# Performance work log

Measured on AMD Instinct MI355X. Metric: run time of the kernel, lower is better.

## Reference

```python
import jax, jax.numpy as jnp
import numpy as np

NBIT = 4          # weight bit-width
GROUP_SIZE = 128  # weight quantization group size (divides k)
HAS_WEIGHT_ZEROS = True


def _quant_dequant_weights(w, group_size=GROUP_SIZE, nbit=NBIT, has_zeros=HAS_WEIGHT_ZEROS):
    # Mirrors torchao _quantize + quantize_per_channel_group, then dequantizes
    # (the native kernel dequantizes inline with the matmul; math is identical).
    qmin = -(1 << (nbit - 1))
    qmax = (1 << (nbit - 1)) - 1
    n, k = w.shape
    g = w.reshape(-1, group_size)                      # [n*k/gs, gs]
    vmin = g.min(axis=1, keepdims=True)
    vmax = g.max(axis=1, keepdims=True)
    scales = (vmax - vmin) / (qmax - qmin)             # per-group scale
    if has_zeros:
        zeros = qmin - jnp.round(vmin / scales)
    else:
        zeros = jnp.zeros_like(scales)
    q = jnp.clip(jnp.round(g / scales) + zeros, qmin, qmax)
    deq = (q - zeros) * scales
    return deq.reshape(n, k)


def _dyn_quant_dequant_act(x):
    # Dynamic per-token (per-row) asymmetric int8 activation quantization.
    qmin, qmax = -128, 127
    xmin = x.min(axis=-1, keepdims=True)
    xmax = x.max(axis=-1, keepdims=True)
    scale = (xmax - xmin) / (qmax - qmin)
    zero = qmin - jnp.round(xmin / scale)
    q = jnp.clip(jnp.round(x / scale) + zero, qmin, qmax)
    return (q - zero) * scale


def setup_inputs() -> dict:
    key = jax.random.key(0)
    k1, k2 = jax.random.split(key)
    x = jax.random.normal(k1, (4, 2048, 4096), dtype=jnp.float32)
    weights = jax.random.normal(k2, (4096, 4096), dtype=jnp.float32) * 0.02
    return {"x": x, "weights": weights}


def reference(x, weights):
    w_deq = _quant_dequant_weights(weights)            # [n, k]
    x_deq = _dyn_quant_dequant_act(x)                  # [..., m, k]
    # y[..., m, n] = x_deq @ w_deq^T
    return jnp.einsum('bmk,nk->bmn', x_deq, w_deq)
```

## Files before the change

kernel.cpp:

```cpp
#include <hip/hip_runtime.h>
#include <hip/hip_bf16.h>
#include <cfloat>

typedef __attribute__((ext_vector_type(8))) short bf16x8;
typedef __attribute__((ext_vector_type(4))) float f32x4;

#define M_DIM 8192
#define N_DIM 4096
#define K_DIM 4096

__device__ inline ushort f2bf(float f) {
    unsigned u = __float_as_uint(f);
    unsigned r = (u + 0x7FFFu + ((u >> 16) & 1u)) >> 16;
    return (ushort)r;
}

#define SWZ(x) ((x) ^ ((((x) >> 7) & 7) << 4))

__global__ __launch_bounds__(256) void w_dequant(const float* __restrict__ w,
                                                 ushort* __restrict__ wq) {
    int g = blockIdx.x * 4 + (threadIdx.x >> 6);
    int lane = threadIdx.x & 63;
    const float* src = w + (size_t)g * 128;
    float2 v = *(const float2*)(src + lane * 2);
    float mn = fminf(v.x, v.y), mx = fmaxf(v.x, v.y);
#pragma unroll
    for (int s = 1; s < 64; s <<= 1) {
        mn = fminf(mn, __shfl_xor(mn, s));
        mx = fmaxf(mx, __shfl_xor(mx, s));
    }
    float scale = (mx - mn) / 15.0f;
    float zero  = -8.0f - rintf(mn / scale);
    float q0 = fminf(fmaxf(rintf(v.x / scale) + zero, -8.0f), 7.0f);
    float q1 = fminf(fmaxf(rintf(v.y / scale) + zero, -8.0f), 7.0f);
    ushort2 o;
    o.x = f2bf((q0 - zero) * scale);
    o.y = f2bf((q1 - zero) * scale);
    *(ushort2*)(wq + (size_t)g * 128 + lane * 2) = o;
}

__global__ __launch_bounds__(256) void act_qdq(const float* __restrict__ x,
                                               ushort* __restrict__ xq) {
    __shared__ float smn[4], smx[4];
    int row = blockIdx.x;
    const float* xr = x + (size_t)row * K_DIM;
    ushort* xo = xq + (size_t)row * K_DIM;
    int t = threadIdx.x;
    float4 v[4];
    float mn = FLT_MAX, mx = -FLT_MAX;
#pragma unroll
    for (int i = 0; i < 4; i++) {
        v[i] = ((const float4*)xr)[t + i * 256];
        mn = fminf(mn, fminf(fminf(v[i].x, v[i].y), fminf(v[i].z, v[i].w)));
        mx = fmaxf(mx, fmaxf(fmaxf(v[i].x, v[i].y), fmaxf(v[i].z, v[i].w)));
    }
#pragma unroll
    for (int s = 1; s < 64; s <<= 1) {
        mn = fminf(mn, __shfl_xor(mn, s));
        mx = fmaxf(mx, __shfl_xor(mx, s));
    }
    int w = t >> 6;
    if ((t & 63) == 0) { smn[w] = mn; smx[w] = mx; }
    __syncthreads();
    mn = fminf(fminf(smn[0], smn[1]), fminf(smn[2], smn[3]));
    mx = fmaxf(fmaxf(smx[0], smx[1]), fmaxf(smx[2], smx[3]));
    float scale = (mx - mn) / 255.0f;
    float zero  = -128.0f - rintf(mn / scale);
#pragma unroll
    for (int i = 0; i < 4; i++) {
        float e0 = v[i].x, e1 = v[i].y, e2 = v[i].z, e3 = v[i].w;
        ushort4 o;
        float q;
        q = fminf(fmaxf(rintf(e0 / scale) + zero, -128.0f), 127.0f); o.x = f2bf((q - zero) * scale);
        q = fminf(fmaxf(rintf(e1 / scale) + zero, -128.0f), 127.0f); o.y = f2bf((q - zero) * scale);
        q = fminf(fmaxf(rintf(e2 / scale) + zero, -128.0f), 127.0f); o.z = f2bf((q - zero) * scale);
        q = fminf(fmaxf(rintf(e3 / scale) + zero, -128.0f), 127.0f); o.w = f2bf((q - zero) * scale);
        ((ushort4*)xo)[t + i * 256] = o;
    }
}

#define BM 256
#define BN 256
#define BK 64
#define NT (K_DIM / BK)
#define HH(T, q) (4 * (T) + (q))

__global__ __launch_bounds__(512, 1) void gemm_bt8(const ushort* __restrict__ A,
                                                   const ushort* __restrict__ B,
                                                   float* __restrict__ C) {
    __shared__ __align__(16) ushort As[2][BM * BK];
    __shared__ __align__(16) ushort Bs[2][BN * BK];

    const int nbx = N_DIM / BN;
    const int nwg = (M_DIM / BM) * nbx;
    int bid = blockIdx.x;
    bid = (bid & 7) * (nwg / 8) + (bid >> 3);
    int mb = bid / nbx, nb = bid % nbx;
    size_t m0 = (size_t)mb * BM, n0 = (size_t)nb * BN;

    const int t = threadIdx.x;
    const int w = t >> 6, lane = t & 63;
    const int wm = w >> 2, wn = w & 3;
    const int lr = lane & 15;
    const int lk = (lane >> 4) << 3;

    const ushort* Ab = A + m0 * K_DIM;
    const ushort* Bb = B + n0 * K_DIM;

    auto STAGE = [&](int h) {
        if (h < 0 || h >= NT * 4) return;
        int T = h >> 2, q = h & 3;
        int d = T & 1;
        ushort* reg = (q < 2) ? As[d] : Bs[d];
        const ushort* gbase = (q < 2) ? Ab : Bb;
        int rhalf = q & 1;
        int k0 = T * BK;
#pragma unroll
        for (int l = 0; l < 2; l++) {
            int base = rhalf * 16384 + (w * 2 + l) * 1024;
            int lb = base + lane * 16;
            int lg = SWZ(lb);
            int r = lg >> 7;
            int c = (lg & 127) >> 1;
            __builtin_amdgcn_global_load_lds(
                (const __attribute__((address_space(1))) unsigned int*)(gbase + (size_t)r * K_DIM + k0 + c),
                (__attribute__((address_space(3))) unsigned int*)((char*)reg + base),
                16, 0, 0);
        }
    };

    f32x4 acc[8][4] = {};
    bf16x8 afr[2][2], bfr[4][2];

#define PHASE(d, q, hA, hB, vm) do {                                              \
    if ((q) == 0) {                                                               \
        _Pragma("unroll") for (int ni = 0; ni < 4; ni++)                          \
        _Pragma("unroll") for (int kk = 0; kk < 2; kk++) {                        \
            int row = wn * 64 + ni * 16 + lr;                                     \
            int lg = row * 128 + (kk * 32 + lk) * 2;                              \
            int pb = SWZ(lg);                                                     \
            bfr[ni][kk] = *(const bf16x8*)((const char*)Bs[d] + pb);              \
        }                                                                         \
    }                                                                             \
    _Pragma("unroll") for (int ii = 0; ii < 2; ii++)                              \
    _Pragma("unroll") for (int kk = 0; kk < 2; kk++) {                            \
        int row = wm * 128 + ((q) * 2 + ii) * 16 + lr;                            \
        int lg = row * 128 + (kk * 32 + lk) * 2;                                  \
        int pb = SWZ(lg);                                                         \
        afr[ii][kk] = *(const bf16x8*)((const char*)As[d] + pb);                  \
    }                                                                             \
    STAGE(hA);                                                                    \
    STAGE(hB);                                                                    \
    __builtin_amdgcn_s_barrier();                                                 \
    asm volatile("s_waitcnt lgkmcnt(0)" ::: "memory");                            \
    __builtin_amdgcn_sched_barrier(0);                                            \
    __builtin_amdgcn_s_setprio(1);                                                \
    _Pragma("unroll") for (int ii = 0; ii < 2; ii++)                              \
    _Pragma("unroll") for (int ni = 0; ni < 4; ni++)                              \
    _Pragma("unroll") for (int kk = 0; kk < 2; kk++)                              \
        acc[(q) * 2 + ii][ni] = __builtin_amdgcn_mfma_f32_16x16x32_bf16(          \
            afr[ii][kk], bfr[ni][kk], acc[(q) * 2 + ii][ni], 0, 0, 0);            \
    __builtin_amdgcn_s_setprio(0);                                                \
    if ((vm) == 1) asm volatile("s_waitcnt vmcnt(4)" ::: "memory");               \
    if ((vm) == 2) asm volatile("s_waitcnt vmcnt(0)" ::: "memory");               \
    __builtin_amdgcn_s_barrier();                                                 \
  } while (0)

    STAGE(HH(0, 0)); STAGE(HH(0, 1)); STAGE(HH(0, 2)); STAGE(HH(0, 3));
    STAGE(HH(1, 2)); STAGE(HH(1, 3));
    asm volatile("s_waitcnt vmcnt(4)" ::: "memory");
    __builtin_amdgcn_s_barrier();

#pragma unroll 1
    for (int i = 0; i < NT / 2 - 1; i++) {
        int T2 = 2 * i;
        PHASE(0, 0, HH(T2 + 1, 0), -1,             0);
        PHASE(0, 1, HH(T2 + 1, 1), HH(T2 + 2, 2),  0);
        PHASE(0, 2, HH(T2 + 2, 3), -1,             0);
        PHASE(0, 3, -1, -1,                        1);
        PHASE(1, 0, HH(T2 + 2, 0), -1,             0);
        PHASE(1, 1, HH(T2 + 2, 1), HH(T2 + 3, 2),  0);
        PHASE(1, 2, HH(T2 + 3, 3), -1,             0);
        PHASE(1, 3, -1, -1,                        1);
    }

    PHASE(0, 0, HH(NT - 1, 0), -1, 0);
    PHASE(0, 1, HH(NT - 1, 1), -1, 0);
    PHASE(0, 2, -1, -1, 0);
    PHASE(0, 3, -1, -1, 2);
    PHASE(1, 0, -1, -1, 0);
    PHASE(1, 1, -1, -1, 0);
    PHASE(1, 2, -1, -1, 0);
    PHASE(1, 3, -1, -1, 0);
#undef PHASE

    int fq = lane >> 4;
#pragma unroll
    for (int mi = 0; mi < 8; mi++) {
#pragma unroll
        for (int ni = 0; ni < 4; ni++) {
#pragma unroll
            for (int r = 0; r < 4; r++) {
                size_t crow = m0 + wm * 128 + mi * 16 + fq * 4 + r;
                C[crow * N_DIM + n0 + wn * 64 + ni * 16 + lr] = acc[mi][ni][r];
            }
        }
    }
}

extern "C" void kernel_launch(void* const* d_in, const int* in_sizes, int n_in,
                              void* d_out, int out_size, void* d_ws, size_t ws_size,
                              hipStream_t stream) {
    const float* x = (const float*)d_in[0];
    const float* w = (const float*)d_in[1];
    float* out = (float*)d_out;

    ushort* wq = (ushort*)d_ws;
    ushort* xq = (ushort*)((char*)d_ws + (size_t)N_DIM * K_DIM * 2);

    hipLaunchKernelGGL(w_dequant, dim3((N_DIM * K_DIM / 128) / 4), dim3(256), 0, stream, w, wq);
    hipLaunchKernelGGL(act_qdq, dim3(M_DIM), dim3(256), 0, stream, x, xq);
    hipLaunchKernelGGL(gemm_bt8, dim3((M_DIM / BM) * (N_DIM / BN)), dim3(512), 0, stream, xq, wq, out);
}
```

Baseline: 330.5 us.

## Re-slice GEMM LDS staging into quarter chunks and interleave A rows across waves

Splits each global-to-LDS tile load into eight smaller chunks (four for A, four for B), issues two of them in every compute phase, and waits with vmcnt at the end of every phase instead of only every fourth one. It also remaps each wave's A rows so that phase q reads a 64-row slab shared by both wave rows, so a phase only depends on the A quarter already loaded. The aim is to spread memory traffic evenly across phases and start MFMA work on partially loaded tiles. The cost is more frequent waitcnt stalls and tighter ordering that could expose load latency.

Measured after the change: 327.1 us. About the same (-1.0%).

```diff
diff --git a/kernel.cpp b/kernel.cpp
--- a/kernel.cpp
+++ b/kernel.cpp
@@ -83,7 +83,6 @@
 #define BN 256
 #define BK 64
 #define NT (K_DIM / BK)
-#define HH(T, q) (4 * (T) + (q))
 
 __global__ __launch_bounds__(512, 1) void gemm_bt8(const ushort* __restrict__ A,
                                                    const ushort* __restrict__ B,
@@ -107,32 +106,28 @@
     const ushort* Ab = A + m0 * K_DIM;
     const ushort* Bb = B + n0 * K_DIM;
 
-    auto STAGE = [&](int h) {
-        if (h < 0 || h >= NT * 4) return;
-        int T = h >> 2, q = h & 3;
+    auto STAGE = [&](int T, int qq) {
+        if (T >= NT) return;
         int d = T & 1;
-        ushort* reg = (q < 2) ? As[d] : Bs[d];
-        const ushort* gbase = (q < 2) ? Ab : Bb;
-        int rhalf = q & 1;
-        int k0 = T * BK;
-#pragma unroll
-        for (int l = 0; l < 2; l++) {
-            int base = rhalf * 16384 + (w * 2 + l) * 1024;
-            int lb = base + lane * 16;
-            int lg = SWZ(lb);
-            int r = lg >> 7;
-            int c = (lg & 127) >> 1;
-            __builtin_amdgcn_global_load_lds(
-                (const __attribute__((address_space(1))) unsigned int*)(gbase + (size_t)r * K_DIM + k0 + c),
-                (__attribute__((address_space(3))) unsigned int*)((char*)reg + base),
-                16, 0, 0);
-        }
+        bool isA = qq < 4;
+        int rq = isA ? qq : qq - 4;
+        ushort* reg = isA ? As[d] : Bs[d];
+        const ushort* gbase = isA ? Ab : Bb;
+        int base = rq * 8192 + w * 1024;
+        int lb = base + lane * 16;
+        int lg = SWZ(lb);
+        int r = lg >> 7;
+        int c = (lg & 127) >> 1;
+        __builtin_amdgcn_global_load_lds(
+            (const __attribute__((address_space(1))) unsigned int*)(gbase + (size_t)r * K_DIM + T * BK + c),
+            (__attribute__((address_space(3))) unsigned int*)((char*)reg + base),
+            16, 0, 0);
     };
 
     f32x4 acc[8][4] = {};
     bf16x8 afr[2][2], bfr[4][2];
 
-#define PHASE(d, q, hA, hB, vm) do {                                              \
+#define PHASE(d, q, sT1, sq1, sT2, sq2, vm) do {                                  \
     if ((q) == 0) {                                                               \
         _Pragma("unroll") for (int ni = 0; ni < 4; ni++)                          \
         _Pragma("unroll") for (int kk = 0; kk < 2; kk++) {                        \
@@ -144,13 +139,13 @@
     }                                                                             \
     _Pragma("unroll") for (int ii = 0; ii < 2; ii++)                              \
     _Pragma("unroll") for (int kk = 0; kk < 2; kk++) {                            \
-        int row = wm * 128 + ((q) * 2 + ii) * 16 + lr;                            \
+        int row = (q) * 64 + wm * 32 + ii * 16 + lr;                              \
         int lg = row * 128 + (kk * 32 + lk) * 2;                                  \
         int pb = SWZ(lg);                                                         \
         afr[ii][kk] = *(const bf16x8*)((const char*)As[d] + pb);                  \
     }                                                                             \
-    STAGE(hA);                                                                    \
-    STAGE(hB);                                                                    \
+    STAGE(sT1, sq1);                                                              \
+    STAGE(sT2, sq2);                                                              \
     __builtin_amdgcn_s_barrier();                                                 \
     asm volatile("s_waitcnt lgkmcnt(0)" ::: "memory");                            \
     __builtin_amdgcn_sched_barrier(0);                                            \
@@ -161,37 +156,39 @@
         acc[(q) * 2 + ii][ni] = __builtin_amdgcn_mfma_f32_16x16x32_bf16(          \
             afr[ii][kk], bfr[ni][kk], acc[(q) * 2 + ii][ni], 0, 0, 0);            \
     __builtin_amdgcn_s_setprio(0);                                                \
-    if ((vm) == 1) asm volatile("s_waitcnt vmcnt(4)" ::: "memory");               \
+    if ((vm) == 1) asm volatile("s_waitcnt vmcnt(8)" ::: "memory");               \
     if ((vm) == 2) asm volatile("s_waitcnt vmcnt(0)" ::: "memory");               \
     __builtin_amdgcn_s_barrier();                                                 \
   } while (0)
 
-    STAGE(HH(0, 0)); STAGE(HH(0, 1)); STAGE(HH(0, 2)); STAGE(HH(0, 3));
-    STAGE(HH(1, 2)); STAGE(HH(1, 3));
-    asm volatile("s_waitcnt vmcnt(4)" ::: "memory");
+    STAGE(0, 0); STAGE(0, 1); STAGE(0, 2); STAGE(0, 3);
+    STAGE(0, 4); STAGE(0, 5); STAGE(0, 6); STAGE(0, 7);
+    STAGE(1, 4); STAGE(1, 5); STAGE(1, 6); STAGE(1, 7);
+    STAGE(1, 0); STAGE(1, 1);
+    asm volatile("s_waitcnt vmcnt(6)" ::: "memory");
     __builtin_amdgcn_s_barrier();
 
 #pragma unroll 1
     for (int i = 0; i < NT / 2 - 1; i++) {
-        int T2 = 2 * i;
-        PHASE(0, 0, HH(T2 + 1, 0), -1,             0);
-        PHASE(0, 1, HH(T2 + 1, 1), HH(T2 + 2, 2),  0);
-        PHASE(0, 2, HH(T2 + 2, 3), -1,             0);
-        PHASE(0, 3, -1, -1,                        1);
-        PHASE(1, 0, HH(T2 + 2, 0), -1,             0);
-        PHASE(1, 1, HH(T2 + 2, 1), HH(T2 + 3, 2),  0);
-        PHASE(1, 2, HH(T2 + 3, 3), -1,             0);
-        PHASE(1, 3, -1, -1,                        1);
-    }
-
-    PHASE(0, 0, HH(NT - 1, 0), -1, 0);
-    PHASE(0, 1, HH(NT - 1, 1), -1, 0);
-    PHASE(0, 2, -1, -1, 0);
-    PHASE(0, 3, -1, -1, 2);
-    PHASE(1, 0, -1, -1, 0);
-    PHASE(1, 1, -1, -1, 0);
-    PHASE(1, 2, -1, -1, 0);
-    PHASE(1, 3, -1, -1, 0);
+        int T0 = 2 * i;
+        PHASE(0, 0, T0 + 1, 2, T0 + 1, 3, 1);
+        PHASE(0, 1, T0 + 2, 4, T0 + 2, 5, 1);
+        PHASE(0, 2, T0 + 2, 6, T0 + 2, 7, 1);
+        PHASE(0, 3, T0 + 2, 0, T0 + 2, 1, 1);
+        PHASE(1, 0, T0 + 2, 2, T0 + 2, 3, 1);
+        PHASE(1, 1, T0 + 3, 4, T0 + 3, 5, 1);
+        PHASE(1, 2, T0 + 3, 6, T0 + 3, 7, 1);
+        PHASE(1, 3, T0 + 3, 0, T0 + 3, 1, 1);
+    }
+
+    PHASE(0, 0, NT - 1, 2, NT - 1, 3, 1);
+    PHASE(0, 1, NT, 0, NT, 0, 1);
+    PHASE(0, 2, NT, 0, NT, 0, 1);
+    PHASE(0, 3, NT, 0, NT, 0, 2);
+    PHASE(1, 0, NT, 0, NT, 0, 0);
+    PHASE(1, 1, NT, 0, NT, 0, 0);
+    PHASE(1, 2, NT, 0, NT, 0, 0);
+    PHASE(1, 3, NT, 0, NT, 0, 0);
 #undef PHASE
 
     int fq = lane >> 4;
@@ -201,7 +198,7 @@
         for (int ni = 0; ni < 4; ni++) {
 #pragma unroll
             for (int r = 0; r < 4; r++) {
-                size_t crow = m0 + wm * 128 + mi * 16 + fq * 4 + r;
+                size_t crow = m0 + (mi >> 1) * 64 + wm * 32 + (mi & 1) * 16 + fq * 4 + r;
                 C[crow * N_DIM + n0 + wn * 64 + ni * 16 + lr] = acc[mi][ni][r];
             }
         }
```
